# Kernel tuning notes

Measured on AMD Instinct MI355X. Metric: run time of the kernel, lower is better.

## Reference

```python
import jax, jax.numpy as jnp
import numpy as np

B, C, L = 8, 64, 65536  # batch, channels, flattened H*W
GN_EPS = 1e-5


def setup_inputs() -> dict:
    key = jax.random.key(0)
    ks = jax.random.split(key, 8)
    return {
        "x": jax.random.normal(ks[0], (B, C, L), dtype=jnp.float32),
        "inj0": jax.random.normal(ks[1], (B, C, L), dtype=jnp.float32),
        "inj1": jax.random.normal(ks[2], (B, C, L), dtype=jnp.float32),
        "residual": jax.random.normal(ks[3], (B, C, L), dtype=jnp.float32),
        "gate_w": jax.random.normal(ks[4], (C, C), dtype=jnp.float32) * (1.0 / np.sqrt(C)),
        "gate_b": jax.random.normal(ks[5], (C,), dtype=jnp.float32) * 0.01,
        "fuse_w": jax.random.normal(ks[6], (C, C), dtype=jnp.float32) * (1.0 / np.sqrt(C)),
        "fuse_b": jax.random.normal(ks[7], (C,), dtype=jnp.float32) * 0.01,
        "gn_w": jnp.ones((C,), dtype=jnp.float32),
        "gn_b": jnp.zeros((C,), dtype=jnp.float32),
    }


def _conv1x1(w, b, t):
    # Conv1d with kernel_size=1: [O,C] x [B,C,L] -> [B,O,L]
    return jnp.einsum('oc,bcl->bol', w, t) + b[None, :, None]


def reference(x, inj0, inj1, residual, gate_w, gate_b, fuse_w, fuse_b, gn_w, gn_b):
    # per-injection gate + elementwise multiply, summed over injections
    acc = jnp.zeros_like(x)
    for inj in (inj0, inj1):  # fixed small list of injection features
        acc = acc + x * _conv1x1(gate_w, gate_b, inj + x)
    # fuse conv + residual + ReLU (dropout p=0 -> identity)
    out = jax.nn.relu(_conv1x1(fuse_w, fuse_b, acc) + residual)
    # GroupNorm(num_groups=1): normalize over (C, L) per sample, per-channel affine
    mean = jnp.mean(out, axis=(1, 2), keepdims=True)
    var = jnp.var(out, axis=(1, 2), keepdims=True)
    out = (out - mean) * jax.lax.rsqrt(var + GN_EPS)
    return out * gn_w[None, :, None] + gn_b[None, :, None]
```

## Files before the change

kernel.cpp:

```cpp
#include <hip/hip_runtime.h>
#include <stdint.h>

#define Bv 8
#define Cv 64
#define Lv 65536
#define TPB 512
#define HALF 128
#define COLS 256
#define BLKS_PER_B (Lv / COLS)
#define GRID1 (Bv * BLKS_PER_B)


typedef __attribute__((ext_vector_type(8))) short short8;
typedef __attribute__((ext_vector_type(4))) float f32x4;

#define SSTRIDE 132

__device__ __forceinline__ uint16_t f2bf(float f) {
    uint32_t u = __float_as_uint(f);
    uint32_t r = u + 0x7FFFu + ((u >> 16) & 1u);
    return (uint16_t)(r >> 16);
}
__device__ __forceinline__ uint32_t pack2bf(float lo, float hi) {
    return (uint32_t)f2bf(lo) | ((uint32_t)f2bf(hi) << 16);
}
__device__ __forceinline__ float bf_lo(uint32_t u) { return __uint_as_float(u << 16); }
__device__ __forceinline__ float bf_hi(uint32_t u) { return __uint_as_float(u & 0xFFFF0000u); }

__global__ void pass1(const float* __restrict__ x, const float* __restrict__ inj0,
                      const float* __restrict__ inj1, const float* __restrict__ resid,
                      const float* __restrict__ gate_w, const float* __restrict__ gate_b,
                      const float* __restrict__ fuse_w, const float* __restrict__ fuse_b,
                      float* __restrict__ out, float* __restrict__ partials)
{
    __shared__ uint32_t s_buf[32 * SSTRIDE];
    __shared__ uint32_t x_buf[32 * SSTRIDE];
    __shared__ uint32_t w_lds[2][64][36];
    __shared__ float cinit[2][64];
    __shared__ float wred[16];

    const int tid  = threadIdx.x;
    const int lane = tid & 63;
    const int w    = tid >> 6;
    const int g    = lane >> 4;
    const int ln   = lane & 15;
    const int n    = 16 * w + ln;

    const int b    = blockIdx.x >> 8;
    const int lb   = blockIdx.x & 255;
    const int bCL  = b * (Cv * Lv);

    {
        const int mat = tid >> 8;
        const int m   = (tid >> 2) & 63;
        const int k0  = (tid & 3) << 4;
        const float* wsrc = mat ? fuse_w : gate_w;
        const float4* w4 = reinterpret_cast<const float4*>(wsrc + m * 64 + k0);
        uint32_t* dst = &w_lds[mat][m][k0 >> 1];
        #pragma unroll
        for (int q = 0; q < 4; ++q) {
            const float4 v = w4[q];
            dst[2 * q]     = pack2bf(v.x, v.y);
            dst[2 * q + 1] = pack2bf(v.z, v.w);
        }
        if (tid < 64) {
            cinit[0][tid] = 2.0f * gate_b[tid];
            cinit[1][tid] = fuse_b[tid];
        }
    }

    float lsum = 0.0f, lsq = 0.0f;

    #pragma unroll 1
    for (int h = 0; h < 2; ++h) {
        const int col0 = lb * COLS + h * HALF;

        #pragma unroll
        for (int uu = 0; uu < 2; ++uu) {
            const int u  = tid + uu * TPB;
            const int kp = u >> 5;
            const int c  = (u & 31) << 2;
            const int rA = bCL + (2 * kp) * Lv + col0 + c;
            const int rB = rA + Lv;
            const float4 xA = *reinterpret_cast<const float4*>(x    + rA);
            const float4 aA = *reinterpret_cast<const float4*>(inj0 + rA);
            const float4 bA = *reinterpret_cast<const float4*>(inj1 + rA);
            const float4 xB = *reinterpret_cast<const float4*>(x    + rB);
            const float4 aB = *reinterpret_cast<const float4*>(inj0 + rB);
            const float4 bB = *reinterpret_cast<const float4*>(inj1 + rB);
            uint4 dw;
            dw.x = pack2bf(aA.x + bA.x + 2.0f * xA.x, aB.x + bB.x + 2.0f * xB.x);
            dw.y = pack2bf(aA.y + bA.y + 2.0f * xA.y, aB.y + bB.y + 2.0f * xB.y);
            dw.z = pack2bf(aA.z + bA.z + 2.0f * xA.z, aB.z + bB.z + 2.0f * xB.z);
            dw.w = pack2bf(aA.w + bA.w + 2.0f * xA.w, aB.w + bB.w + 2.0f * xB.w);
            *reinterpret_cast<uint4*>(&s_buf[kp * SSTRIDE + c]) = dw;
            uint4 dx;
            dx.x = pack2bf(xA.x, xB.x);
            dx.y = pack2bf(xA.y, xB.y);
            dx.z = pack2bf(xA.z, xB.z);
            dx.w = pack2bf(xA.w, xB.w);
            *reinterpret_cast<uint4*>(&x_buf[kp * SSTRIDE + c]) = dx;
        }
        __syncthreads();

        f32x4 D1[4];
        #pragma unroll
        for (int oc = 0; oc < 4; ++oc) {
            const float4 cb = *reinterpret_cast<const float4*>(&cinit[0][16 * oc + 4 * g]);
            D1[oc][0] = cb.x; D1[oc][1] = cb.y; D1[oc][2] = cb.z; D1[oc][3] = cb.w;
        }
        {
            uint4 B0, B1;
            B0.x = s_buf[(4 * g + 0) * SSTRIDE + n];
            B0.y = s_buf[(4 * g + 1) * SSTRIDE + n];
            B0.z = s_buf[(4 * g + 2) * SSTRIDE + n];
            B0.w = s_buf[(4 * g + 3) * SSTRIDE + n];
            B1.x = s_buf[(16 + 4 * g + 0) * SSTRIDE + n];
            B1.y = s_buf[(16 + 4 * g + 1) * SSTRIDE + n];
            B1.z = s_buf[(16 + 4 * g + 2) * SSTRIDE + n];
            B1.w = s_buf[(16 + 4 * g + 3) * SSTRIDE + n];
            #pragma unroll
            for (int oc = 0; oc < 4; ++oc) {
                const int m = ln + 16 * oc;
                const uint4 A0 = *reinterpret_cast<const uint4*>(&w_lds[0][m][4 * g]);
                const uint4 A1 = *reinterpret_cast<const uint4*>(&w_lds[0][m][16 + 4 * g]);
                D1[oc] = __builtin_amdgcn_mfma_f32_16x16x32_bf16(
                    __builtin_bit_cast(short8, A0), __builtin_bit_cast(short8, B0),
                    D1[oc], 0, 0, 0);
                D1[oc] = __builtin_amdgcn_mfma_f32_16x16x32_bf16(
                    __builtin_bit_cast(short8, A1), __builtin_bit_cast(short8, B1),
                    D1[oc], 0, 0, 0);
            }
        }

        #pragma unroll
        for (int oc = 0; oc < 4; ++oc) {
            const int kp = 8 * oc + 2 * g;
            const uint32_t u0 = x_buf[kp * SSTRIDE + n];
            const uint32_t u1 = x_buf[(kp + 1) * SSTRIDE + n];
            float av[4];
            av[0] = bf_lo(u0) * D1[oc][0];
            av[1] = bf_hi(u0) * D1[oc][1];
            av[2] = bf_lo(u1) * D1[oc][2];
            av[3] = bf_hi(u1) * D1[oc][3];
            s_buf[kp * SSTRIDE + n]       = pack2bf(av[0], av[1]);
            s_buf[(kp + 1) * SSTRIDE + n] = pack2bf(av[2], av[3]);
        }
        __syncthreads();

        f32x4 D2[4];
        #pragma unroll
        for (int oc = 0; oc < 4; ++oc) {
            const float4 cb = *reinterpret_cast<const float4*>(&cinit[1][16 * oc + 4 * g]);
            D2[oc][0] = cb.x; D2[oc][1] = cb.y; D2[oc][2] = cb.z; D2[oc][3] = cb.w;
        }
        {
            uint4 B0, B1;
            B0.x = s_buf[(4 * g + 0) * SSTRIDE + n];
            B0.y = s_buf[(4 * g + 1) * SSTRIDE + n];
            B0.z = s_buf[(4 * g + 2) * SSTRIDE + n];
            B0.w = s_buf[(4 * g + 3) * SSTRIDE + n];
            B1.x = s_buf[(16 + 4 * g + 0) * SSTRIDE + n];
            B1.y = s_buf[(16 + 4 * g + 1) * SSTRIDE + n];
            B1.z = s_buf[(16 + 4 * g + 2) * SSTRIDE + n];
            B1.w = s_buf[(16 + 4 * g + 3) * SSTRIDE + n];
            #pragma unroll
            for (int oc = 0; oc < 4; ++oc) {
                const int m = ln + 16 * oc;
                const uint4 A0 = *reinterpret_cast<const uint4*>(&w_lds[1][m][4 * g]);
                const uint4 A1 = *reinterpret_cast<const uint4*>(&w_lds[1][m][16 + 4 * g]);
                D2[oc] = __builtin_amdgcn_mfma_f32_16x16x32_bf16(
                    __builtin_bit_cast(short8, A0), __builtin_bit_cast(short8, B0),
                    D2[oc], 0, 0, 0);
                D2[oc] = __builtin_amdgcn_mfma_f32_16x16x32_bf16(
                    __builtin_bit_cast(short8, A1), __builtin_bit_cast(short8, B1),
                    D2[oc], 0, 0, 0);
            }
        }
        __syncthreads();

        {
            float* uf = reinterpret_cast<float*>(s_buf);
            const int rowin = tid >> 4;
            const int cl    = tid & 15;
            #pragma unroll 1
            for (int ck = 0; ck < 2; ++ck) {
                #pragma unroll
                for (int oc2 = 0; oc2 < 2; ++oc2) {
                    const int oc = 2 * ck + oc2;
                    #pragma unroll
                    for (int j = 0; j < 4; ++j)
                        uf[(16 * oc2 + 4 * g + j) * SSTRIDE + n] = D2[oc][j];
                }
                const int m   = 32 * ck + rowin;
                const int gbm = bCL + m * Lv + col0;
                const float4 ra = *reinterpret_cast<const float4*>(&resid[gbm + 4 * cl]);
                const float4 rb = *reinterpret_cast<const float4*>(&resid[gbm + 4 * cl + 64]);
                __syncthreads();
                float4 va = *reinterpret_cast<const float4*>(&uf[rowin * SSTRIDE + 4 * cl]);
                float4 vb = *reinterpret_cast<const float4*>(&uf[rowin * SSTRIDE + 4 * cl + 64]);
                va.x = fmaxf(va.x + ra.x, 0.0f); va.y = fmaxf(va.y + ra.y, 0.0f);
                va.z = fmaxf(va.z + ra.z, 0.0f); va.w = fmaxf(va.w + ra.w, 0.0f);
                vb.x = fmaxf(vb.x + rb.x, 0.0f); vb.y = fmaxf(vb.y + rb.y, 0.0f);
                vb.z = fmaxf(vb.z + rb.z, 0.0f); vb.w = fmaxf(vb.w + rb.w, 0.0f);
                *reinterpret_cast<float4*>(&out[gbm + 4 * cl])      = va;
                *reinterpret_cast<float4*>(&out[gbm + 4 * cl + 64]) = vb;
                lsum += (va.x + va.y) + (va.z + va.w) + (vb.x + vb.y) + (vb.z + vb.w);
                lsq = fmaf(va.x, va.x, lsq); lsq = fmaf(va.y, va.y, lsq);
                lsq = fmaf(va.z, va.z, lsq); lsq = fmaf(va.w, va.w, lsq);
                lsq = fmaf(vb.x, vb.x, lsq); lsq = fmaf(vb.y, vb.y, lsq);
                lsq = fmaf(vb.z, vb.z, lsq); lsq = fmaf(vb.w, vb.w, lsq);
                __syncthreads();
            }
        }
    }

    #pragma unroll
    for (int st = 1; st < 64; st <<= 1) {
        lsum += __shfl_xor(lsum, st);
        lsq  += __shfl_xor(lsq,  st);
    }
    if (lane == 0) { wred[2 * w] = lsum; wred[2 * w + 1] = lsq; }
    __syncthreads();
    if (tid == 0) {
        float s = 0.0f, q = 0.0f;
        #pragma unroll
        for (int i = 0; i < 8; ++i) { s += wred[2 * i]; q += wred[2 * i + 1]; }
        partials[2 * blockIdx.x]     = s;
        partials[2 * blockIdx.x + 1] = q;
    }
}

__global__ __launch_bounds__(256)
void pass2(const float* __restrict__ partials, const float* __restrict__ gn_w,
           const float* __restrict__ gn_b, float* __restrict__ sb)
{
    __shared__ float r1[256], r2[256];
    __shared__ float mean_s, rs_s;
    const int b = blockIdx.x, tid = threadIdx.x;
    r1[tid] = partials[2 * (b * 256 + tid)];
    r2[tid] = partials[2 * (b * 256 + tid) + 1];
    __syncthreads();
    #pragma unroll
    for (int st = 128; st > 0; st >>= 1) {
        if (tid < st) { r1[tid] += r1[tid + st]; r2[tid] += r2[tid + st]; }
        __syncthreads();
    }
    if (tid == 0) {
        const float n = (float)Cv * (float)Lv;
        const float mean = r1[0] / n;
        const float var  = r2[0] / n - mean * mean;
        mean_s = mean;
        rs_s   = rsqrtf(var + 1e-5f);
    }
    __syncthreads();
    if (tid < Cv) {
        const float sc = gn_w[tid] * rs_s;
        sb[b * Cv + tid]           = sc;
        sb[Bv * Cv + b * Cv + tid] = fmaf(-mean_s, sc, gn_b[tid]);
    }
}

__global__ __launch_bounds__(256)
void pass3(float* __restrict__ out, const float* __restrict__ sb)
{
    const int total4 = (Bv * Cv * Lv) / 4;
    for (int i = blockIdx.x * blockDim.x + threadIdx.x; i < total4;
         i += gridDim.x * blockDim.x) {
        const int row = i >> 14;
        const float sc = sb[row];
        const float bi = sb[Bv * Cv + row];
        float4 v = reinterpret_cast<float4*>(out)[i];
        v.x = fmaf(v.x, sc, bi);
        v.y = fmaf(v.y, sc, bi);
        v.z = fmaf(v.z, sc, bi);
        v.w = fmaf(v.w, sc, bi);
        reinterpret_cast<float4*>(out)[i] = v;
    }
}

extern "C" void kernel_launch(void* const* d_in, const int* in_sizes, int n_in,
                              void* d_out, int out_size, void* d_ws, size_t ws_size,
                              hipStream_t stream)
{
    const float* x      = (const float*)d_in[0];
    const float* inj0   = (const float*)d_in[1];
    const float* inj1   = (const float*)d_in[2];
    const float* resid  = (const float*)d_in[3];
    const float* gate_w = (const float*)d_in[4];
    const float* gate_b = (const float*)d_in[5];
    const float* fuse_w = (const float*)d_in[6];
    const float* fuse_b = (const float*)d_in[7];
    const float* gn_w   = (const float*)d_in[8];
    const float* gn_b   = (const float*)d_in[9];

    float* out      = (float*)d_out;
    float* ws       = (float*)d_ws;
    float* partials = ws;
    float* sb       = ws + 2 * GRID1;

    hipLaunchKernelGGL(pass1, dim3(GRID1), dim3(TPB), 0, stream,
                       x, inj0, inj1, resid, gate_w, gate_b, fuse_w, fuse_b,
                       out, partials);
    hipLaunchKernelGGL(pass2, dim3(Bv), dim3(256), 0, stream,
                       partials, gn_w, gn_b, sb);
    hipLaunchKernelGGL(pass3, dim3(2048), dim3(256), 0, stream, out, sb);
}
```

Baseline: 184.6 us.

## Prefetch second half-tile inputs into registers during first half compute

Loads the second 128-column half's x/inj0/inj1 values into registers at the start of the first half iteration, then packs them into LDS after the first half finishes. The aim is to overlap global memory latency with the MFMA and epilogue work of the first half. In exchange it holds 48 extra floats per thread, which raises register pressure and may lower occupancy. It also depends on the existing trailing barrier in the epilogue so that the LDS buffers are not overwritten while still being read.

```diff
diff --git a/kernel.cpp b/kernel.cpp
--- a/kernel.cpp
+++ b/kernel.cpp
@@ -50,6 +50,11 @@
     const int lb   = blockIdx.x & 255;
     const int bCL  = b * (Cv * Lv);
 
+    const int kp0 = tid >> 5;
+    const int c0s = (tid & 31) << 2;
+    const int kp1 = (tid + TPB) >> 5;
+    const int c1s = ((tid + TPB) & 31) << 2;
+
     {
         const int mat = tid >> 8;
         const int m   = (tid >> 2) & 63;
@@ -69,17 +74,12 @@
         }
     }
 
-    float lsum = 0.0f, lsq = 0.0f;
-
-    #pragma unroll 1
-    for (int h = 0; h < 2; ++h) {
-        const int col0 = lb * COLS + h * HALF;
-
+    {
+        const int col0 = lb * COLS;
         #pragma unroll
         for (int uu = 0; uu < 2; ++uu) {
-            const int u  = tid + uu * TPB;
-            const int kp = u >> 5;
-            const int c  = (u & 31) << 2;
+            const int kp = uu ? kp1 : kp0;
+            const int c  = uu ? c1s : c0s;
             const int rA = bCL + (2 * kp) * Lv + col0 + c;
             const int rB = rA + Lv;
             const float4 xA = *reinterpret_cast<const float4*>(x    + rA);
@@ -88,20 +88,44 @@
             const float4 xB = *reinterpret_cast<const float4*>(x    + rB);
             const float4 aB = *reinterpret_cast<const float4*>(inj0 + rB);
             const float4 bB = *reinterpret_cast<const float4*>(inj1 + rB);
-            uint4 dw;
+            uint4 dw, dx;
             dw.x = pack2bf(aA.x + bA.x + 2.0f * xA.x, aB.x + bB.x + 2.0f * xB.x);
             dw.y = pack2bf(aA.y + bA.y + 2.0f * xA.y, aB.y + bB.y + 2.0f * xB.y);
             dw.z = pack2bf(aA.z + bA.z + 2.0f * xA.z, aB.z + bB.z + 2.0f * xB.z);
             dw.w = pack2bf(aA.w + bA.w + 2.0f * xA.w, aB.w + bB.w + 2.0f * xB.w);
             *reinterpret_cast<uint4*>(&s_buf[kp * SSTRIDE + c]) = dw;
-            uint4 dx;
             dx.x = pack2bf(xA.x, xB.x);
             dx.y = pack2bf(xA.y, xB.y);
             dx.z = pack2bf(xA.z, xB.z);
             dx.w = pack2bf(xA.w, xB.w);
             *reinterpret_cast<uint4*>(&x_buf[kp * SSTRIDE + c]) = dx;
         }
-        __syncthreads();
+    }
+    __syncthreads();
+
+    float lsum = 0.0f, lsq = 0.0f;
+    float4 L[2][6];
+
+    #pragma unroll 1
+    for (int h = 0; h < 2; ++h) {
+        const int col0 = lb * COLS + h * HALF;
+
+        if (h == 0) {
+            const int col1 = lb * COLS + HALF;
+            #pragma unroll
+            for (int uu = 0; uu < 2; ++uu) {
+                const int kp = uu ? kp1 : kp0;
+                const int c  = uu ? c1s : c0s;
+                const int rA = bCL + (2 * kp) * Lv + col1 + c;
+                const int rB = rA + Lv;
+                L[uu][0] = *reinterpret_cast<const float4*>(x    + rA);
+                L[uu][1] = *reinterpret_cast<const float4*>(inj0 + rA);
+                L[uu][2] = *reinterpret_cast<const float4*>(inj1 + rA);
+                L[uu][3] = *reinterpret_cast<const float4*>(x    + rB);
+                L[uu][4] = *reinterpret_cast<const float4*>(inj0 + rB);
+                L[uu][5] = *reinterpret_cast<const float4*>(inj1 + rB);
+            }
+        }
 
         f32x4 D1[4];
         #pragma unroll
@@ -213,6 +237,28 @@
                 __syncthreads();
             }
         }
+
+        if (h == 0) {
+            #pragma unroll
+            for (int uu = 0; uu < 2; ++uu) {
+                const int kp = uu ? kp1 : kp0;
+                const int c  = uu ? c1s : c0s;
+                const float4 xA = L[uu][0], aA = L[uu][1], bA = L[uu][2];
+                const float4 xB = L[uu][3], aB = L[uu][4], bB = L[uu][5];
+                uint4 dw, dx;
+                dw.x = pack2bf(aA.x + bA.x + 2.0f * xA.x, aB.x + bB.x + 2.0f * xB.x);
+                dw.y = pack2bf(aA.y + bA.y + 2.0f * xA.y, aB.y + bB.y + 2.0f * xB.y);
+                dw.z = pack2bf(aA.z + bA.z + 2.0f * xA.z, aB.z + bB.z + 2.0f * xB.z);
+                dw.w = pack2bf(aA.w + bA.w + 2.0f * xA.w, aB.w + bB.w + 2.0f * xB.w);
+                *reinterpret_cast<uint4*>(&s_buf[kp * SSTRIDE + c]) = dw;
+                dx.x = pack2bf(xA.x, xB.x);
+                dx.y = pack2bf(xA.y, xB.y);
+                dx.z = pack2bf(xA.z, xB.z);
+                dx.w = pack2bf(xA.w, xB.w);
+                *reinterpret_cast<uint4*>(&x_buf[kp * SSTRIDE + c]) = dx;
+            }
+            __syncthreads();
+        }
     }
 
     #pragma unroll
```

New measurement: 215.7 us. +16.8%, slower.
